# Performance work log

Hardware: AMD Instinct MI355X
Metric: run time of the kernel (lower is better)

The kernel has to match this reference:

```python
import jax, jax.numpy as jnp
import numpy as np

FP8_MAX = 448.0  # torch.finfo(float8_e4m3fn).max
TINY = float(np.finfo(np.float32).tiny)
BN = BK = 128  # block sizes


def _make_fp8_weight(key, N, K):
    """Mirror _create_fp8_weight: per-128x128-block scales, fp8 quantized values."""
    w = jax.random.normal(key, (N, K), jnp.float32) * 0.01
    wb = w.reshape(N // BN, BN, K // BK, BK)
    amax = jnp.abs(wb).max(axis=(1, 3))
    scale_inv = jnp.maximum(amax / FP8_MAX, TINY)  # [N/BN, K/BK]
    wq = (wb / scale_inv[:, None, :, None]).reshape(N, K)
    wq = wq.astype(jnp.float8_e4m3fn).astype(jnp.float32)  # fp8-rounded values
    return wq, scale_inv


def _dequant(wq, scale_inv):
    N, K = wq.shape
    nb, kb = scale_inv.shape
    wb = wq.reshape(nb, N // nb, kb, K // kb) * scale_inv[:, None, :, None]
    return wb.reshape(N, K)


def setup_inputs() -> dict:
    key = jax.random.key(0)
    kx, k1, k2, k3 = jax.random.split(key, 4)
    T, H, F = 4096, 2048, 7168  # tokens, hidden_dim, ffn_dim
    x = jax.random.normal(kx, (T, H), jnp.float32)
    w1_q, w1_s = _make_fp8_weight(k1, F, H)
    w3_q, w3_s = _make_fp8_weight(k3, F, H)
    w2_q, w2_s = _make_fp8_weight(k2, H, F)
    return {"hidden_states": x, "w1_q": w1_q, "w1_s": w1_s,
            "w3_q": w3_q, "w3_s": w3_s, "w2_q": w2_q, "w2_s": w2_s}


def reference(hidden_states, w1_q, w1_s, w3_q, w3_s, w2_q, w2_s):
    x = hidden_states
    w1 = _dequant(w1_q, w1_s)  # [F, H]
    w3 = _dequant(w3_q, w3_s)  # [F, H]
    w2 = _dequant(w2_q, w2_s)  # [H, F]
    g = x @ w1.T               # [T, F]
    u = x @ w3.T               # [T, F]
    fused = jax.nn.silu(g) * u
    return fused @ w2.T        # [T, H]
```

## Files before the change

kernel.cpp:

```cpp
#include <hip/hip_runtime.h>
#include <stdint.h>

typedef __attribute__((ext_vector_type(8))) short short8;
typedef __attribute__((ext_vector_type(4))) float floatx4;

__device__ __forceinline__ unsigned short f2bf(float f) {
  union { float f; unsigned int u; } c; c.f = f;
  unsigned int u = c.u;
  unsigned int r = (u + 0x7fffu + ((u >> 16) & 1u)) >> 16;
  return (unsigned short)r;
}
__device__ __forceinline__ float bf2f(unsigned short h) {
  union { unsigned int u; float f; } c; c.u = ((unsigned int)h) << 16;
  return c.f;
}

__device__ __forceinline__ void load16_to_lds(const void* g, void* l) {
  __builtin_amdgcn_global_load_lds(
      (const __attribute__((address_space(1))) unsigned int*)g,
      (__attribute__((address_space(3))) unsigned int*)l, 16, 0, 0);
}

__global__ void f32_to_bf16_kernel(const float* __restrict__ in,
                                   unsigned short* __restrict__ out, long n4) {
  long i = blockIdx.x * (long)blockDim.x + threadIdx.x;
  if (i >= n4) return;
  float4 v = ((const float4*)in)[i];
  ushort4 o;
  o.x = f2bf(v.x); o.y = f2bf(v.y); o.z = f2bf(v.z); o.w = f2bf(v.w);
  ((ushort4*)out)[i] = o;
}

__global__ void dequant2_kernel(const float* __restrict__ w1q,
                                const float* __restrict__ s1,
                                const float* __restrict__ w3q,
                                const float* __restrict__ s3,
                                unsigned short* __restrict__ o1,
                                unsigned short* __restrict__ o3,
                                int K, int sK) {
  int n = blockIdx.y;
  int k = blockIdx.x * 1024 + threadIdx.x * 4;
  size_t idx = (size_t)n * K + k;
  int sidx = (n >> 7) * sK + (k >> 7);
  float sc1 = s1[sidx], sc3 = s3[sidx];
  float4 v1 = *(const float4*)(w1q + idx);
  float4 v3 = *(const float4*)(w3q + idx);
  ushort4 a, b;
  a.x = f2bf(v1.x * sc1); a.y = f2bf(v1.y * sc1);
  a.z = f2bf(v1.z * sc1); a.w = f2bf(v1.w * sc1);
  b.x = f2bf(v3.x * sc3); b.y = f2bf(v3.y * sc3);
  b.z = f2bf(v3.z * sc3); b.w = f2bf(v3.w * sc3);
  *(ushort4*)(o1 + idx) = a;
  *(ushort4*)(o3 + idx) = b;
}

__global__ void dequant1_kernel(const float* __restrict__ wq,
                                const float* __restrict__ s,
                                unsigned short* __restrict__ out,
                                int K, int sK) {
  int n = blockIdx.y;
  int k = blockIdx.x * 1024 + threadIdx.x * 4;
  size_t idx = (size_t)n * K + k;
  float sc = s[(n >> 7) * sK + (k >> 7)];
  float4 v = *(const float4*)(wq + idx);
  ushort4 o;
  o.x = f2bf(v.x * sc); o.y = f2bf(v.y * sc);
  o.z = f2bf(v.z * sc); o.w = f2bf(v.w * sc);
  *(ushort4*)(out + idx) = o;
}


__global__ __launch_bounds__(256, 2) void dual_gemm_silu(
    const unsigned short* __restrict__ A,
    const unsigned short* __restrict__ B1,
    const unsigned short* __restrict__ B3,
    unsigned short* __restrict__ C,
    int M, int N, int K) {
  __shared__ unsigned short As[128 * 64];
  __shared__ unsigned short B1s[128 * 64];
  __shared__ unsigned short B3s[128 * 64];

  const int tid = threadIdx.x;
  const int lane = tid & 63;
  const int wave = tid >> 6;
  const int wm = wave >> 1;
  const int wn = wave & 1;
  const int m0 = blockIdx.y * 128, n0 = blockIdx.x * 128;

  int soff[4];
  int sdst[4];
#pragma unroll
  for (int p = 0; p < 4; p++) {
    int u = tid + 256 * p;
    int r = u >> 3;
    int c = ((u & 7) ^ (r & 7)) * 8;
    soff[p] = r * K + c;
    sdst[p] = u * 8;
  }

  const int q = lane >> 4;
  const int r16 = lane & 15;
  const int rx = r16 & 7;

  floatx4 acc_g[4][4], acc_u[4][4];
#pragma unroll
  for (int i = 0; i < 4; i++)
#pragma unroll
    for (int j = 0; j < 4; j++) {
      acc_g[i][j] = (floatx4){0.f, 0.f, 0.f, 0.f};
      acc_u[i][j] = (floatx4){0.f, 0.f, 0.f, 0.f};
    }

  const unsigned short* Abase = A + (size_t)m0 * K;
  const unsigned short* B1base = B1 + (size_t)n0 * K;
  const unsigned short* B3base = B3 + (size_t)n0 * K;

  for (int k0 = 0; k0 < K; k0 += 64) {
#pragma unroll
    for (int p = 0; p < 4; p++) {
      load16_to_lds(Abase + soff[p] + k0, &As[sdst[p]]);
      load16_to_lds(B1base + soff[p] + k0, &B1s[sdst[p]]);
      load16_to_lds(B3base + soff[p] + k0, &B3s[sdst[p]]);
    }
    __syncthreads();

#pragma unroll
    for (int kh = 0; kh < 2; kh++) {
      const int kq = kh * 4 + q;
      short8 a[4], b1v[4], b3v[4];
#pragma unroll
      for (int t = 0; t < 4; t++) {
        int row = wm * 64 + t * 16 + r16;
        a[t] = *(const short8*)&As[(row * 8 + (kq ^ rx)) * 8];
      }
#pragma unroll
      for (int j = 0; j < 4; j++) {
        int row = wn * 64 + j * 16 + r16;
        int u = (row * 8 + (kq ^ rx)) * 8;
        b1v[j] = *(const short8*)&B1s[u];
        b3v[j] = *(const short8*)&B3s[u];
      }
#pragma unroll
      for (int i = 0; i < 4; i++)
#pragma unroll
        for (int j = 0; j < 4; j++) {
          acc_g[i][j] = __builtin_amdgcn_mfma_f32_16x16x32_bf16(
              a[i], b1v[j], acc_g[i][j], 0, 0, 0);
          acc_u[i][j] = __builtin_amdgcn_mfma_f32_16x16x32_bf16(
              a[i], b3v[j], acc_u[i][j], 0, 0, 0);
        }
    }
    __syncthreads();
  }

#pragma unroll
  for (int i = 0; i < 4; i++) {
    int row0 = m0 + wm * 64 + i * 16 + q * 4;
#pragma unroll
    for (int j = 0; j < 4; j++) {
      int col = n0 + wn * 64 + j * 16 + r16;
#pragma unroll
      for (int rr = 0; rr < 4; rr++) {
        float gv = acc_g[i][j][rr];
        float uv = acc_u[i][j][rr];
        float sv = gv / (1.f + __expf(-gv)) * uv;
        C[(size_t)(row0 + rr) * N + col] = f2bf(sv);
      }
    }
  }
}

__global__ __launch_bounds__(256, 2) void gemm_nt_f32_4w(
    const unsigned short* __restrict__ A,
    const unsigned short* __restrict__ B,
    float* __restrict__ C,
    int M, int N, int K) {
  __shared__ unsigned short As[128 * 64];
  __shared__ unsigned short Bs[128 * 64];

  const int tid = threadIdx.x;
  const int lane = tid & 63;
  const int wave = tid >> 6;
  const int wm = wave >> 1;
  const int wn = wave & 1;
  const int m0 = blockIdx.y * 128, n0 = blockIdx.x * 128;

  int soff[4], sdst[4];
#pragma unroll
  for (int p = 0; p < 4; p++) {
    int u = tid + 256 * p;
    int r = u >> 3;
    int c = ((u & 7) ^ (r & 7)) * 8;
    soff[p] = r * K + c;
    sdst[p] = u * 8;
  }

  const int q = lane >> 4;
  const int r16 = lane & 15;
  const int rx = r16 & 7;

  floatx4 acc[4][4];
#pragma unroll
  for (int i = 0; i < 4; i++)
#pragma unroll
    for (int j = 0; j < 4; j++) acc[i][j] = (floatx4){0.f, 0.f, 0.f, 0.f};

  const unsigned short* Abase = A + (size_t)m0 * K;
  const unsigned short* Bbase = B + (size_t)n0 * K;

  for (int k0 = 0; k0 < K; k0 += 64) {
#pragma unroll
    for (int p = 0; p < 4; p++) {
      load16_to_lds(Abase + soff[p] + k0, &As[sdst[p]]);
      load16_to_lds(Bbase + soff[p] + k0, &Bs[sdst[p]]);
    }
    __syncthreads();

#pragma unroll
    for (int kh = 0; kh < 2; kh++) {
      const int kq = kh * 4 + q;
      short8 a[4], b[4];
#pragma unroll
      for (int t = 0; t < 4; t++) {
        int row = wm * 64 + t * 16 + r16;
        a[t] = *(const short8*)&As[(row * 8 + (kq ^ rx)) * 8];
      }
#pragma unroll
      for (int j = 0; j < 4; j++) {
        int row = wn * 64 + j * 16 + r16;
        b[j] = *(const short8*)&Bs[(row * 8 + (kq ^ rx)) * 8];
      }
#pragma unroll
      for (int i = 0; i < 4; i++)
#pragma unroll
        for (int j = 0; j < 4; j++)
          acc[i][j] = __builtin_amdgcn_mfma_f32_16x16x32_bf16(
              a[i], b[j], acc[i][j], 0, 0, 0);
    }
    __syncthreads();
  }

#pragma unroll
  for (int i = 0; i < 4; i++) {
    int row0 = m0 + wm * 64 + i * 16 + q * 4;
#pragma unroll
    for (int j = 0; j < 4; j++) {
      int col = n0 + wn * 64 + j * 16 + r16;
#pragma unroll
      for (int rr = 0; rr < 4; rr++)
        C[(size_t)(row0 + rr) * N + col] = acc[i][j][rr];
    }
  }
}

extern "C" void kernel_launch(void* const* d_in, const int* in_sizes, int n_in,
                              void* d_out, int out_size, void* d_ws, size_t ws_size,
                              hipStream_t stream) {
  const float* x = (const float*)d_in[0];
  const float* w1q = (const float*)d_in[1];
  const float* w1s = (const float*)d_in[2];
  const float* w3q = (const float*)d_in[3];
  const float* w3s = (const float*)d_in[4];
  const float* w2q = (const float*)d_in[5];
  const float* w2s = (const float*)d_in[6];

  const int T = 4096, H = 2048, F = 7168;

  char* ws = (char*)d_ws;
  unsigned short* xb  = (unsigned short*)ws;  ws += (size_t)T * H * 2;
  unsigned short* w1b = (unsigned short*)ws;  ws += (size_t)F * H * 2;
  unsigned short* w3b = (unsigned short*)ws;  ws += (size_t)F * H * 2;
  unsigned short* w2b = (unsigned short*)ws;  ws += (size_t)H * F * 2;
  unsigned short* g   = (unsigned short*)ws;  ws += (size_t)T * F * 2;

  long xn4 = (long)T * H / 4;

  f32_to_bf16_kernel<<<(xn4 + 255) / 256, 256, 0, stream>>>(x, xb, xn4);
  dequant2_kernel<<<dim3(H / 1024, F), 256, 0, stream>>>(
      w1q, w1s, w3q, w3s, w1b, w3b, H, H / 128);
  dequant1_kernel<<<dim3(F / 1024, H), 256, 0, stream>>>(
      w2q, w2s, w2b, F, F / 128);

  dual_gemm_silu<<<dim3(F / 128, T / 128), 256, 0, stream>>>(xb, w1b, w3b, g, T, F, H);

  gemm_nt_f32_4w<<<dim3(H / 128, T / 128), 256, 0, stream>>>(g, w2b, (float*)d_out, T, H, F);
}
```

Measured before the change: 578.1 us.

## Widen down-projection GEMM tile to 128x256 and split K in two

The final GEMM now uses a 128x256 output tile, so each wave covers 64x128 and every A fragment feeds more MFMAs. To keep the block count unchanged, K is split into two halves across blockIdx.z. One half writes straight to the output and the other writes to a partial buffer that reuses the no-longer-needed xb/w1b workspace. A separate elementwise kernel then adds the partial into the output. This costs an extra pass over the 32MB output, plus higher register pressure and more LDS per block.

```diff
diff --git a/kernel.cpp b/kernel.cpp
--- a/kernel.cpp
+++ b/kernel.cpp
@@ -9,10 +9,6 @@
   unsigned int u = c.u;
   unsigned int r = (u + 0x7fffu + ((u >> 16) & 1u)) >> 16;
   return (unsigned short)r;
-}
-__device__ __forceinline__ float bf2f(unsigned short h) {
-  union { unsigned int u; float f; } c; c.u = ((unsigned int)h) << 16;
-  return c.f;
 }
 
 __device__ __forceinline__ void load16_to_lds(const void* g, void* l) {
@@ -69,7 +65,6 @@
   *(ushort4*)(out + idx) = o;
 }
 
-
 __global__ __launch_bounds__(256, 2) void dual_gemm_silu(
     const unsigned short* __restrict__ A,
     const unsigned short* __restrict__ B1,
@@ -170,87 +165,110 @@
   }
 }
 
-__global__ __launch_bounds__(256, 2) void gemm_nt_f32_4w(
+__global__ __launch_bounds__(256, 2) void gemm_nt_dc(
     const unsigned short* __restrict__ A,
     const unsigned short* __restrict__ B,
-    float* __restrict__ C,
-    int M, int N, int K) {
+    float* __restrict__ Cout,
+    float* __restrict__ Cpart,
+    int M, int N, int Ktot, int kLen) {
   __shared__ unsigned short As[128 * 64];
-  __shared__ unsigned short Bs[128 * 64];
+  __shared__ unsigned short Bs[256 * 64];
 
   const int tid = threadIdx.x;
   const int lane = tid & 63;
   const int wave = tid >> 6;
   const int wm = wave >> 1;
   const int wn = wave & 1;
-  const int m0 = blockIdx.y * 128, n0 = blockIdx.x * 128;
-
-  int soff[4], sdst[4];
+  const int m0 = blockIdx.y * 128, n0 = blockIdx.x * 256;
+  const int kOff = blockIdx.z * kLen;
+
+  int soffA[4], sdstA[4];
 #pragma unroll
   for (int p = 0; p < 4; p++) {
     int u = tid + 256 * p;
     int r = u >> 3;
     int c = ((u & 7) ^ (r & 7)) * 8;
-    soff[p] = r * K + c;
-    sdst[p] = u * 8;
+    soffA[p] = r * Ktot + c;
+    sdstA[p] = u * 8;
+  }
+  int soffB[8], sdstB[8];
+#pragma unroll
+  for (int p = 0; p < 8; p++) {
+    int u = tid + 256 * p;
+    int r = u >> 3;
+    int c = ((u & 7) ^ (r & 7)) * 8;
+    soffB[p] = r * Ktot + c;
+    sdstB[p] = u * 8;
   }
 
   const int q = lane >> 4;
   const int r16 = lane & 15;
   const int rx = r16 & 7;
 
-  floatx4 acc[4][4];
+  floatx4 acc[4][8];
 #pragma unroll
   for (int i = 0; i < 4; i++)
 #pragma unroll
-    for (int j = 0; j < 4; j++) acc[i][j] = (floatx4){0.f, 0.f, 0.f, 0.f};
-
-  const unsigned short* Abase = A + (size_t)m0 * K;
-  const unsigned short* Bbase = B + (size_t)n0 * K;
-
-  for (int k0 = 0; k0 < K; k0 += 64) {
-#pragma unroll
-    for (int p = 0; p < 4; p++) {
-      load16_to_lds(Abase + soff[p] + k0, &As[sdst[p]]);
-      load16_to_lds(Bbase + soff[p] + k0, &Bs[sdst[p]]);
-    }
+    for (int j = 0; j < 8; j++) acc[i][j] = (floatx4){0.f, 0.f, 0.f, 0.f};
+
+  const unsigned short* Abase = A + (size_t)m0 * Ktot + kOff;
+  const unsigned short* Bbase = B + (size_t)n0 * Ktot + kOff;
+
+  for (int k0 = 0; k0 < kLen; k0 += 64) {
+#pragma unroll
+    for (int p = 0; p < 4; p++)
+      load16_to_lds(Abase + soffA[p] + k0, &As[sdstA[p]]);
+#pragma unroll
+    for (int p = 0; p < 8; p++)
+      load16_to_lds(Bbase + soffB[p] + k0, &Bs[sdstB[p]]);
     __syncthreads();
 
 #pragma unroll
     for (int kh = 0; kh < 2; kh++) {
       const int kq = kh * 4 + q;
-      short8 a[4], b[4];
+      short8 a[4], b[8];
 #pragma unroll
       for (int t = 0; t < 4; t++) {
         int row = wm * 64 + t * 16 + r16;
         a[t] = *(const short8*)&As[(row * 8 + (kq ^ rx)) * 8];
       }
 #pragma unroll
-      for (int j = 0; j < 4; j++) {
-        int row = wn * 64 + j * 16 + r16;
+      for (int j = 0; j < 8; j++) {
+        int row = wn * 128 + j * 16 + r16;
         b[j] = *(const short8*)&Bs[(row * 8 + (kq ^ rx)) * 8];
       }
 #pragma unroll
       for (int i = 0; i < 4; i++)
 #pragma unroll
-        for (int j = 0; j < 4; j++)
+        for (int j = 0; j < 8; j++)
           acc[i][j] = __builtin_amdgcn_mfma_f32_16x16x32_bf16(
               a[i], b[j], acc[i][j], 0, 0, 0);
     }
     __syncthreads();
   }
 
+  float* C = (blockIdx.z == 0) ? Cout : Cpart;
 #pragma unroll
   for (int i = 0; i < 4; i++) {
     int row0 = m0 + wm * 64 + i * 16 + q * 4;
 #pragma unroll
-    for (int j = 0; j < 4; j++) {
-      int col = n0 + wn * 64 + j * 16 + r16;
+    for (int j = 0; j < 8; j++) {
+      int col = n0 + wn * 128 + j * 16 + r16;
 #pragma unroll
       for (int rr = 0; rr < 4; rr++)
         C[(size_t)(row0 + rr) * N + col] = acc[i][j][rr];
     }
   }
+}
+
+__global__ void add_f32_kernel(float* __restrict__ out,
+                               const float* __restrict__ p1, long n4) {
+  long i = blockIdx.x * (long)blockDim.x + threadIdx.x;
+  if (i >= n4) return;
+  float4 a = ((const float4*)out)[i];
+  float4 b = ((const float4*)p1)[i];
+  a.x += b.x; a.y += b.y; a.z += b.z; a.w += b.w;
+  ((float4*)out)[i] = a;
 }
 
 extern "C" void kernel_launch(void* const* d_in, const int* in_sizes, int n_in,
@@ -272,6 +290,7 @@
   unsigned short* w3b = (unsigned short*)ws;  ws += (size_t)F * H * 2;
   unsigned short* w2b = (unsigned short*)ws;  ws += (size_t)H * F * 2;
   unsigned short* g   = (unsigned short*)ws;  ws += (size_t)T * F * 2;
+  float* part1 = (float*)xb;
 
   long xn4 = (long)T * H / 4;
 
@@ -283,5 +302,9 @@
 
   dual_gemm_silu<<<dim3(F / 128, T / 128), 256, 0, stream>>>(xb, w1b, w3b, g, T, F, H);
 
-  gemm_nt_f32_4w<<<dim3(H / 128, T / 128), 256, 0, stream>>>(g, w2b, (float*)d_out, T, H, F);
-}
+  gemm_nt_dc<<<dim3(H / 256, T / 128, 2), 256, 0, stream>>>(
+      g, w2b, (float*)d_out, part1, T, H, F, F / 2);
+
+  long on4 = (long)T * H / 4;
+  add_f32_kernel<<<(on4 + 255) / 256, 256, 0, stream>>>((float*)d_out, part1, on4);
+}
```

Result: slower. 600.1 us (+3.8%).
